# Kernel optimization log

Hardware: AMD Instinct MI355X
Metric: run time of the kernel (lower is better)

The kernel has to match this reference:

```python
import jax, jax.numpy as jnp
import numpy as np

NUM_HEADS = 16
ALPHA = 1.0          # attention_logits_alpha
SOFTCAP = 50.0       # logit_softcapping


def setup_inputs() -> dict:
    key = jax.random.key(0)
    ks = jax.random.split(key, 7)
    B, S, E = 2, 2048, 2048
    mk = lambda k, shape, sc=1.0: jax.random.normal(k, shape, dtype=jnp.float32) * sc
    return {
        "q": mk(ks[0], (B, S, E)),
        "k": mk(ks[1], (B, S, E)),
        "v": mk(ks[2], (B, S, E)),
        # nn.Linear weights are [out, in]; xavier-ish scale 1/sqrt(E)
        "Wq": mk(ks[3], (E, E), E ** -0.5),
        "Wk": mk(ks[4], (E, E), E ** -0.5),
        "Wv": mk(ks[5], (E, E), E ** -0.5),
        "Wo": mk(ks[6], (E, E), E ** -0.5),
    }


def reference(q, k, v, Wq, Wk, Wv, Wo):
    B, S, E = q.shape
    H = NUM_HEADS
    D = E // H  # head_dim = 128

    def split_heads(x):  # [B,S,E] -> [B,H,S,D]
        return x.reshape(B, S, H, D).transpose(0, 2, 1, 3)

    qh = split_heads(q @ Wq.T)  # q_projection_scale = 1.0
    kh = split_heads(k @ Wk.T)
    vh = split_heads(v @ Wv.T)

    # scaled_dot_product: scale q by 1/sqrt(head_dim)
    qh = qh * (D ** -0.5)
    logits = ALPHA * jnp.einsum("bhqd,bhkd->bhqk", qh, kh)
    # logit softcapping: cap * tanh(logits / cap)
    logits = SOFTCAP * jnp.tanh(logits / SOFTCAP)
    # fp32 softmax (softmax_dtype_fp32=True)
    probs = jax.nn.softmax(logits.astype(jnp.float32), axis=-1).astype(qh.dtype)
    # dropout rate 0.0 -> identity
    ctx = jnp.einsum("bhqk,bhkd->bhqd", probs, vh)
    ctx = ctx.transpose(0, 2, 1, 3).reshape(B, S, E)
    return ctx @ Wo.T  # output_projection_scale = 1.0
```

## Files before the change

### kernel.cpp

```cpp
#include <hip/hip_runtime.h>
#include <hip/hip_bf16.h>
#include <stdint.h>


typedef __attribute__((ext_vector_type(8))) short s16x8;
typedef __attribute__((ext_vector_type(4))) float f32x4;

typedef const __attribute__((address_space(1))) char* gcptr;
typedef __attribute__((address_space(3))) char* lcptr;

#define MFMA_BF16(a, b, c) __builtin_amdgcn_mfma_f32_16x16x32_bf16((a), (b), (c), 0, 0, 0)

__device__ __forceinline__ short f2bf(float f) {
  union { float f; unsigned u; } x; x.f = f;
  unsigned r = (x.u + 0x7fffu + ((x.u >> 16) & 1u)) >> 16;
  return (short)r;
}

__device__ __forceinline__ void gload16(const void* g, void* lds) {
  __builtin_amdgcn_global_load_lds((gcptr)g, (lcptr)lds, 16, 0, 0);
}

constexpr int GK = 2048;
constexpr int SL = 2048, EMB = 2048, HD = 128;

__global__ void cvt_all(const float* __restrict__ q, const float* __restrict__ k,
                        const float* __restrict__ v, const float* __restrict__ wq,
                        const float* __restrict__ wk, const float* __restrict__ wv,
                        const float* __restrict__ wo, short* __restrict__ dst) {
  const int N8A = 1 << 20, N8W = 1 << 19;
  const int total = 3 * N8A + 4 * N8W;
  int i = blockIdx.x * blockDim.x + threadIdx.x;
  int stride = gridDim.x * blockDim.x;
  for (; i < total; i += stride) {
    const float* src;
    size_t loc;
    if (i < 3 * N8A) {
      int sel = i >> 20;
      loc = (size_t)(i & (N8A - 1));
      src = sel == 0 ? q : (sel == 1 ? k : v);
    } else {
      int w = i - 3 * N8A;
      int sel = w >> 19;
      loc = (size_t)(w & (N8W - 1));
      src = sel == 0 ? wq : (sel == 1 ? wk : (sel == 2 ? wv : wo));
    }
    f32x4 a = *reinterpret_cast<const f32x4*>(src + loc * 8);
    f32x4 b = *reinterpret_cast<const f32x4*>(src + loc * 8 + 4);
    s16x8 w8;
#pragma unroll
    for (int j = 0; j < 4; ++j) { w8[j] = f2bf(a[j]); w8[4 + j] = f2bf(b[j]); }
    *reinterpret_cast<s16x8*>(dst + (size_t)i * 8) = w8;
  }
}

__global__ __launch_bounds__(256, 2)
void gemm_qkv(const short* __restrict__ a0, const short* __restrict__ a1,
              const short* __restrict__ w0, const short* __restrict__ w1,
              const short* __restrict__ w2, const short* __restrict__ a2,
              short* __restrict__ o0, short* __restrict__ o1,
              short* __restrict__ o2) {
  __shared__ __align__(16) short As[128 * 64];
  __shared__ __align__(16) short Bs[128 * 64];
  const int z = blockIdx.z;
  const short* A = z == 0 ? a0 : (z == 1 ? a1 : w2);
  const short* B = z == 0 ? w0 : (z == 1 ? w1 : a2);
  short* C = z == 0 ? o0 : (z == 1 ? o1 : o2);
  const int bm = z == 2 ? blockIdx.x : blockIdx.y;
  const int bn = z == 2 ? blockIdx.y : blockIdx.x;
  const int gn = z == 2 ? 4096 : 2048;

  const int tid = threadIdx.x;
  const int lane = tid & 63;
  const int wid = tid >> 6;
  const int wr = wid >> 1, wc = wid & 1;
  const int g = lane >> 4, r = lane & 15;

  const f32x4 fz = {0.f, 0.f, 0.f, 0.f};
  f32x4 acc[4][4];
#pragma unroll
  for (int m = 0; m < 4; ++m)
#pragma unroll
    for (int n = 0; n < 4; ++n) acc[m][n] = fz;

  const short* Ab = A + (size_t)bm * 128 * GK;
  const short* Bb = B + (size_t)bn * 128 * GK;

  for (int kt = 0; kt < GK; kt += 64) {
#pragma unroll
    for (int i = 0; i < 4; ++i) {
      int c = i * 256 + tid;
      int row = c >> 3, c8 = c & 7;
      gload16(Ab + (size_t)row * GK + kt + c8 * 8, As + c * 8);
      gload16(Bb + (size_t)row * GK + kt + c8 * 8, Bs + c * 8);
    }
    __syncthreads();
#pragma unroll
    for (int kk = 0; kk < 2; ++kk) {
      s16x8 af[4], bf[4];
#pragma unroll
      for (int m = 0; m < 4; ++m)
        af[m] = *reinterpret_cast<const s16x8*>(As + (wr * 64 + m * 16 + r) * 64 + kk * 32 + g * 8);
#pragma unroll
      for (int n = 0; n < 4; ++n)
        bf[n] = *reinterpret_cast<const s16x8*>(Bs + (wc * 64 + n * 16 + r) * 64 + kk * 32 + g * 8);
#pragma unroll
      for (int m = 0; m < 4; ++m)
#pragma unroll
        for (int n = 0; n < 4; ++n) acc[m][n] = MFMA_BF16(af[m], bf[n], acc[m][n]);
    }
    __syncthreads();
  }

#pragma unroll
  for (int m = 0; m < 4; ++m)
#pragma unroll
    for (int j = 0; j < 4; ++j) {
      int crow = bm * 128 + wr * 64 + m * 16 + g * 4 + j;
      size_t off = (size_t)crow * gn + bn * 128 + wc * 64 + r;
#pragma unroll
      for (int n = 0; n < 4; ++n) C[off + n * 16] = f2bf(acc[m][n][j]);
    }
}

__global__ __launch_bounds__(256, 2)
void gemm_out(const short* __restrict__ A, const short* __restrict__ B,
              float* __restrict__ C) {
  __shared__ __align__(16) short As[128 * 64];
  __shared__ __align__(16) short Bs[128 * 64];
  const int tid = threadIdx.x;
  const int lane = tid & 63;
  const int wid = tid >> 6;
  const int wr = wid >> 1, wc = wid & 1;
  const int g = lane >> 4, r = lane & 15;
  const int bm = blockIdx.y, bn = blockIdx.x;

  const f32x4 fz = {0.f, 0.f, 0.f, 0.f};
  f32x4 acc[4][4];
#pragma unroll
  for (int m = 0; m < 4; ++m)
#pragma unroll
    for (int n = 0; n < 4; ++n) acc[m][n] = fz;

  const short* Ab = A + (size_t)bm * 128 * GK;
  const short* Bb = B + (size_t)bn * 128 * GK;

  for (int kt = 0; kt < GK; kt += 64) {
#pragma unroll
    for (int i = 0; i < 4; ++i) {
      int c = i * 256 + tid;
      int row = c >> 3, c8 = c & 7;
      gload16(Ab + (size_t)row * GK + kt + c8 * 8, As + c * 8);
      gload16(Bb + (size_t)row * GK + kt + c8 * 8, Bs + c * 8);
    }
    __syncthreads();
#pragma unroll
    for (int kk = 0; kk < 2; ++kk) {
      s16x8 af[4], bf[4];
#pragma unroll
      for (int m = 0; m < 4; ++m)
        af[m] = *reinterpret_cast<const s16x8*>(As + (wr * 64 + m * 16 + r) * 64 + kk * 32 + g * 8);
#pragma unroll
      for (int n = 0; n < 4; ++n)
        bf[n] = *reinterpret_cast<const s16x8*>(Bs + (wc * 64 + n * 16 + r) * 64 + kk * 32 + g * 8);
#pragma unroll
      for (int m = 0; m < 4; ++m)
#pragma unroll
        for (int n = 0; n < 4; ++n) acc[m][n] = MFMA_BF16(af[m], bf[n], acc[m][n]);
    }
    __syncthreads();
  }

#pragma unroll
  for (int m = 0; m < 4; ++m)
#pragma unroll
    for (int j = 0; j < 4; ++j) {
      int crow = bm * 128 + wr * 64 + m * 16 + g * 4 + j;
      size_t off = (size_t)crow * 2048 + bn * 128 + wc * 64 + r;
#pragma unroll
      for (int n = 0; n < 4; ++n) C[off + n * 16] = acc[m][n][j];
    }
}

__global__ __launch_bounds__(256, 1)
void attn(const short* __restrict__ Q, const short* __restrict__ K,
          const short* __restrict__ VT, short* __restrict__ O) {
  __shared__ __align__(16) short Ks[128 * 128];
  __shared__ __align__(16) short Vt[128 * 128];
  __shared__ __align__(16) short Ps[4 * 2 * 16 * 136];

  const int tid = threadIdx.x;
  const int lane = tid & 63;
  const int wid = tid >> 6;
  const int g = lane >> 4, r = lane & 15;

  const int dflat = blockIdx.x + (blockIdx.y << 4);
  const int cflat = ((dflat & 7) << 6) + (dflat >> 3);
  const int qb = cflat & 15;
  const int bh = cflat >> 4;
  const int b = bh >> 4, h = bh & 15;
  const size_t base = (size_t)b * SL * EMB + (size_t)h * HD;
  const size_t vbase = (size_t)h * HD * 4096 + (size_t)b * SL;

  const int q0 = qb * 128 + wid * 32;
  s16x8 qf[2][4];
#pragma unroll
  for (int s = 0; s < 2; ++s)
#pragma unroll
    for (int kk = 0; kk < 4; ++kk)
      qf[s][kk] = *reinterpret_cast<const s16x8*>(
          Q + base + (size_t)(q0 + s * 16 + r) * EMB + kk * 32 + g * 8);

  const f32x4 fz = {0.f, 0.f, 0.f, 0.f};
  float l_run[2][4];
  f32x4 acc_o[2][8];
#pragma unroll
  for (int s = 0; s < 2; ++s) {
#pragma unroll
    for (int i = 0; i < 4; ++i) l_run[s][i] = 0.f;
#pragma unroll
    for (int i = 0; i < 8; ++i) acc_o[s][i] = fz;
  }

  const float SCALE = 0.08838834764831845f;
  const float C50I = 0.02f;
  const float CA = -1.f / 3.f, CB = 2.f / 15.f;

  const int n0 = (wid << 6) + lane;
  auto stageK = [&](int t) {
    const int kv0 = t * 128;
#pragma unroll
    for (int i = 0; i < 8; ++i) {
      int n = n0 + i * 256;
      int rr = n >> 4, ch = n & 15;
      int lch = ch ^ (rr & 7);
      gload16(K + base + (size_t)(kv0 + rr) * EMB + lch * 8, Ks + n * 8);
    }
  };
  auto stageV = [&](int t) {
    const int kv0 = t * 128;
#pragma unroll
    for (int i = 0; i < 8; ++i) {
      int n = n0 + i * 256;
      int rr = n >> 4, ch = n & 15;
      int lch = ch ^ (rr & 7);
      gload16(VT + vbase + (size_t)rr * 4096 + kv0 + lch * 8, Vt + n * 8);
    }
  };

  stageK(0);
  stageV(0);

  const int psb = (wid * 2) * 16 * 136;

  for (int t = 0; t < SL / 128; ++t) {
    asm volatile("s_waitcnt vmcnt(8)" ::: "memory");
    __builtin_amdgcn_s_barrier();

    f32x4 sv[2][8];
#pragma unroll
    for (int kn = 0; kn < 8; ++kn) {
      sv[0][kn] = fz; sv[1][kn] = fz;
#pragma unroll
      for (int kk = 0; kk < 4; ++kk) {
        const s16x8 kf = *reinterpret_cast<const s16x8*>(
            Ks + ((kn * 16 + r) * 16 + ((kk * 4 + g) ^ (r & 7))) * 8);
        sv[0][kn] = MFMA_BF16(qf[0][kk], kf, sv[0][kn]);
        sv[1][kn] = MFMA_BF16(qf[1][kk], kf, sv[1][kn]);
      }
    }
    asm volatile("s_waitcnt lgkmcnt(0)" ::: "memory");
    __builtin_amdgcn_s_barrier();
    stageK((t + 1) & 15);

#pragma unroll
    for (int s = 0; s < 2; ++s)
#pragma unroll
      for (int kn = 0; kn < 8; ++kn)
#pragma unroll
        for (int reg = 0; reg < 4; ++reg) {
          float z = sv[s][kn][reg] * SCALE;
          float x = z * C50I;
          float x2 = x * x;
          float poly = __builtin_fmaf(x2, __builtin_fmaf(x2, CB, CA), 1.f);
          float cap = fminf(z * poly, 50.f);
          float pe = __expf(cap - 50.f);
          l_run[s][reg] += pe;
          Ps[psb + s * 16 * 136 + (g * 4 + reg) * 136 + kn * 16 + r] = f2bf(pe);
        }

    asm volatile("s_waitcnt vmcnt(8)" ::: "memory");
    __builtin_amdgcn_s_barrier();

#pragma unroll
    for (int c = 0; c < 4; ++c) {
      const s16x8 pa0 = *reinterpret_cast<const s16x8*>(
          Ps + psb + 0 * 16 * 136 + r * 136 + c * 32 + g * 8);
      const s16x8 pa1 = *reinterpret_cast<const s16x8*>(
          Ps + psb + 1 * 16 * 136 + r * 136 + c * 32 + g * 8);
#pragma unroll
      for (int dn = 0; dn < 8; ++dn) {
        const int d = dn * 16 + r;
        const s16x8 vf = *reinterpret_cast<const s16x8*>(
            Vt + (d * 16 + ((c * 4 + g) ^ (r & 7))) * 8);
        acc_o[0][dn] = MFMA_BF16(pa0, vf, acc_o[0][dn]);
        acc_o[1][dn] = MFMA_BF16(pa1, vf, acc_o[1][dn]);
      }
    }
    asm volatile("s_waitcnt lgkmcnt(0)" ::: "memory");
    __builtin_amdgcn_s_barrier();
    stageV((t + 1) & 15);
  }

  asm volatile("s_waitcnt vmcnt(0)" ::: "memory");

#pragma unroll
  for (int s = 0; s < 2; ++s) {
#pragma unroll
    for (int reg = 0; reg < 4; ++reg) {
#pragma unroll
      for (int off = 1; off < 16; off <<= 1)
        l_run[s][reg] += __shfl_xor(l_run[s][reg], off);
      l_run[s][reg] = 1.f / l_run[s][reg];
    }
#pragma unroll
    for (int dn = 0; dn < 8; ++dn)
#pragma unroll
      for (int reg = 0; reg < 4; ++reg) {
        int row = q0 + s * 16 + g * 4 + reg;
        O[base + (size_t)row * EMB + dn * 16 + r] = f2bf(acc_o[s][dn][reg] * l_run[s][reg]);
      }
  }
}

__global__ void fill_f32(float* p, int n, float val) {
  int i = blockIdx.x * blockDim.x + threadIdx.x;
  if (i < n) p[i] = val;
}

extern "C" void kernel_launch(void* const* d_in, const int* in_sizes, int n_in,
                              void* d_out, int out_size, void* d_ws, size_t ws_size,
                              hipStream_t stream) {
  const float* q  = (const float*)d_in[0];
  const float* k  = (const float*)d_in[1];
  const float* v  = (const float*)d_in[2];
  const float* wq = (const float*)d_in[3];
  const float* wk = (const float*)d_in[4];
  const float* wv = (const float*)d_in[5];
  const float* wo = (const float*)d_in[6];
  float* out = (float*)d_out;

  bool ok = (n_in == 7) && out_size == 8388608;
  for (int i = 0; i < 3 && ok; ++i) ok = (in_sizes[i] == 8388608);
  for (int i = 3; i < 7 && ok; ++i) ok = (in_sizes[i] == 4194304);
  if (!ok) {
    fill_f32<<<(out_size + 255) / 256, 256, 0, stream>>>(out, out_size, 150.f);
    return;
  }

  const size_t NA = 8388608;
  const size_t NW = 4194304;
  const size_t need = (3 * NA + 4 * NW + 4 * NA) * sizeof(short);
  if (ws_size < need) {
    fill_f32<<<(out_size + 255) / 256, 256, 0, stream>>>(out, out_size, 128.f);
    return;
  }

  short* bq  = (short*)d_ws;
  short* bk  = bq + NA;
  short* bv  = bk + NA;
  short* bwq = bv + NA;
  short* bwk = bwq + NW;
  short* bwv = bwk + NW;
  short* bwo = bwv + NW;
  short* Qp  = bwo + NW;
  short* Kp  = Qp + NA;
  short* VpT = Kp + NA;
  short* Cx  = VpT + NA;

  dim3 blk(256);
  dim3 g3(16, 32, 3);
  dim3 gg(16, 32);
  dim3 ga(16, 32);

  cvt_all<<<2048, 256, 0, stream>>>(q, k, v, wq, wk, wv, wo, bq);
  gemm_qkv<<<g3, blk, 0, stream>>>(bq, bk, bwq, bwk, bwv, bv, Qp, Kp, VpT);
  attn<<<ga, blk, 0, stream>>>(Qp, Kp, VpT, Cx);
  gemm_out<<<gg, blk, 0, stream>>>(Cx, bwo, out);
}
```

Measured before the change: 378.9 us.

## Halve attention KV tile, stage through registers, raise occupancy to two blocks

Shrinks the attention kernel's KV tile from 128 to 64 keys and cuts shared memory usage, so launch bounds can allow two blocks per CU. It replaces the asynchronous global-to-LDS loads with a register-prefetch double buffer (global to registers, then registers to LDS), padding rows instead of swizzling K. Removes the custom vmcnt/barrier pipeline in favour of plain __syncthreads. The goal is more latency hiding through occupancy. In exchange there are twice as many loop iterations and barriers, plus more register pressure from the prefetch registers.

```diff
diff --git a/kernel.cpp b/kernel.cpp
--- a/kernel.cpp
+++ b/kernel.cpp
@@ -182,12 +182,12 @@
     }
 }
 
-__global__ __launch_bounds__(256, 1)
+__global__ __launch_bounds__(256, 2)
 void attn(const short* __restrict__ Q, const short* __restrict__ K,
           const short* __restrict__ VT, short* __restrict__ O) {
-  __shared__ __align__(16) short Ks[128 * 128];
-  __shared__ __align__(16) short Vt[128 * 128];
-  __shared__ __align__(16) short Ps[4 * 2 * 16 * 136];
+  __shared__ __align__(16) short Ks[64 * 136];
+  __shared__ __align__(16) short Vt[128 * 72];
+  __shared__ __align__(16) short Ps[4][2][16 * 72];
 
   const int tid = threadIdx.x;
   const int lane = tid & 63;
@@ -226,57 +226,50 @@
   const float C50I = 0.02f;
   const float CA = -1.f / 3.f, CB = 2.f / 15.f;
 
-  const int n0 = (wid << 6) + lane;
-  auto stageK = [&](int t) {
-    const int kv0 = t * 128;
-#pragma unroll
-    for (int i = 0; i < 8; ++i) {
-      int n = n0 + i * 256;
-      int rr = n >> 4, ch = n & 15;
-      int lch = ch ^ (rr & 7);
-      gload16(K + base + (size_t)(kv0 + rr) * EMB + lch * 8, Ks + n * 8);
-    }
-  };
-  auto stageV = [&](int t) {
-    const int kv0 = t * 128;
-#pragma unroll
-    for (int i = 0; i < 8; ++i) {
-      int n = n0 + i * 256;
-      int rr = n >> 4, ch = n & 15;
-      int lch = ch ^ (rr & 7);
-      gload16(VT + vbase + (size_t)rr * 4096 + kv0 + lch * 8, Vt + n * 8);
-    }
-  };
-
-  stageK(0);
-  stageV(0);
-
-  const int psb = (wid * 2) * 16 * 136;
-
-  for (int t = 0; t < SL / 128; ++t) {
-    asm volatile("s_waitcnt vmcnt(8)" ::: "memory");
-    __builtin_amdgcn_s_barrier();
-
-    f32x4 sv[2][8];
-#pragma unroll
-    for (int kn = 0; kn < 8; ++kn) {
+  const int rk = tid >> 4, ck = tid & 15;
+  const int rv = tid >> 3, cv = tid & 7;
+  const int cvx = cv ^ (rv & 7);
+  s16x8 kreg[4], vreg[4];
+#pragma unroll
+  for (int i = 0; i < 4; ++i) {
+    kreg[i] = *reinterpret_cast<const s16x8*>(K + base + (size_t)(rk + i * 16) * EMB + ck * 8);
+    vreg[i] = *reinterpret_cast<const s16x8*>(VT + vbase + (size_t)(rv + i * 32) * 4096 + cv * 8);
+  }
+
+  for (int t = 0; t < SL / 64; ++t) {
+    __syncthreads();
+#pragma unroll
+    for (int i = 0; i < 4; ++i) {
+      *reinterpret_cast<s16x8*>(&Ks[(rk + i * 16) * 136 + ck * 8]) = kreg[i];
+      *reinterpret_cast<s16x8*>(&Vt[(rv + i * 32) * 72 + (cvx << 3)]) = vreg[i];
+    }
+    __syncthreads();
+
+    if (t + 1 < SL / 64) {
+      const int kv1 = (t + 1) * 64;
+#pragma unroll
+      for (int i = 0; i < 4; ++i) {
+        kreg[i] = *reinterpret_cast<const s16x8*>(K + base + (size_t)(kv1 + rk + i * 16) * EMB + ck * 8);
+        vreg[i] = *reinterpret_cast<const s16x8*>(VT + vbase + (size_t)(rv + i * 32) * 4096 + kv1 + cv * 8);
+      }
+    }
+
+    f32x4 sv[2][4];
+#pragma unroll
+    for (int kn = 0; kn < 4; ++kn) {
       sv[0][kn] = fz; sv[1][kn] = fz;
 #pragma unroll
       for (int kk = 0; kk < 4; ++kk) {
-        const s16x8 kf = *reinterpret_cast<const s16x8*>(
-            Ks + ((kn * 16 + r) * 16 + ((kk * 4 + g) ^ (r & 7))) * 8);
+        s16x8 kf = *reinterpret_cast<const s16x8*>(&Ks[(kn * 16 + r) * 136 + kk * 32 + g * 8]);
         sv[0][kn] = MFMA_BF16(qf[0][kk], kf, sv[0][kn]);
         sv[1][kn] = MFMA_BF16(qf[1][kk], kf, sv[1][kn]);
       }
     }
-    asm volatile("s_waitcnt lgkmcnt(0)" ::: "memory");
-    __builtin_amdgcn_s_barrier();
-    stageK((t + 1) & 15);
 
 #pragma unroll
     for (int s = 0; s < 2; ++s)
 #pragma unroll
-      for (int kn = 0; kn < 8; ++kn)
+      for (int kn = 0; kn < 4; ++kn)
 #pragma unroll
         for (int reg = 0; reg < 4; ++reg) {
           float z = sv[s][kn][reg] * SCALE;
@@ -286,33 +279,31 @@
           float cap = fminf(z * poly, 50.f);
           float pe = __expf(cap - 50.f);
           l_run[s][reg] += pe;
-          Ps[psb + s * 16 * 136 + (g * 4 + reg) * 136 + kn * 16 + r] = f2bf(pe);
+          sv[s][kn][reg] = pe;
         }
 
-    asm volatile("s_waitcnt vmcnt(8)" ::: "memory");
-    __builtin_amdgcn_s_barrier();
-
-#pragma unroll
-    for (int c = 0; c < 4; ++c) {
-      const s16x8 pa0 = *reinterpret_cast<const s16x8*>(
-          Ps + psb + 0 * 16 * 136 + r * 136 + c * 32 + g * 8);
-      const s16x8 pa1 = *reinterpret_cast<const s16x8*>(
-          Ps + psb + 1 * 16 * 136 + r * 136 + c * 32 + g * 8);
+#pragma unroll
+    for (int s = 0; s < 2; ++s)
+#pragma unroll
+      for (int kn = 0; kn < 4; ++kn)
+#pragma unroll
+        for (int reg = 0; reg < 4; ++reg)
+          Ps[wid][s][(g * 4 + reg) * 72 + kn * 16 + r] = f2bf(sv[s][kn][reg]);
+
+#pragma unroll
+    for (int c = 0; c < 2; ++c) {
+      s16x8 pa0 = *reinterpret_cast<const s16x8*>(&Ps[wid][0][r * 72 + c * 32 + g * 8]);
+      s16x8 pa1 = *reinterpret_cast<const s16x8*>(&Ps[wid][1][r * 72 + c * 32 + g * 8]);
 #pragma unroll
       for (int dn = 0; dn < 8; ++dn) {
-        const int d = dn * 16 + r;
-        const s16x8 vf = *reinterpret_cast<const s16x8*>(
-            Vt + (d * 16 + ((c * 4 + g) ^ (r & 7))) * 8);
+        int d = dn * 16 + r;
+        int pc = ((c * 4 + g) ^ (r & 7));
+        s16x8 vf = *reinterpret_cast<const s16x8*>(&Vt[d * 72 + (pc << 3)]);
         acc_o[0][dn] = MFMA_BF16(pa0, vf, acc_o[0][dn]);
         acc_o[1][dn] = MFMA_BF16(pa1, vf, acc_o[1][dn]);
       }
     }
-    asm volatile("s_waitcnt lgkmcnt(0)" ::: "memory");
-    __builtin_amdgcn_s_barrier();
-    stageV((t + 1) & 15);
-  }
-
-  asm volatile("s_waitcnt vmcnt(0)" ::: "memory");
+  }
 
 #pragma unroll
   for (int s = 0; s < 2; ++s) {
```

After: 339.8 us. 1.12x faster.
